# Performance work log

Hardware: AMD Instinct MI355X
Metric: run time of the kernel (lower is better)

## Reference

```python
import jax, jax.numpy as jnp
import numpy as np
from jax import lax

B = 64          # batch
L = 8192        # seq_len
NB = 20         # n_pha_bands + n_amp_bands
K = 769         # padded FIR kernel length (odd), ~cycle*fs/low_hz for lowest band


def setup_inputs() -> dict:
    key = jax.random.key(0)
    kx, kk = jax.random.split(key)
    x = jax.random.normal(kx, (B, 1, L), dtype=jnp.float32)
    # stand-in for the designed+padded tensorpac FIR bank (registered buffer)
    kernels = jax.random.normal(kk, (NB, K), dtype=jnp.float32) * (1.0 / K)
    return {"x": x, "kernels": kernels}


def reference(x, kernels):
    # filtfilt_mode=True, edge_mode=None branch of BandPassFilter.forward
    nb, k = kernels.shape
    seq_len = x.shape[-1]
    padlen = min(3 * k, seq_len - 1)  # same for all bands: kernels share padded length
    xs = x[:, 0, :]  # [B, L]
    # scipy-style odd extension, vectorized over batch (replaces per-sample loop)
    left = -jnp.flip(xs[:, 1:padlen + 1], axis=-1)
    right = -jnp.flip(xs[:, -padlen - 1:-1], axis=-1)
    xp = jnp.concatenate([left, xs, right], axis=-1)[:, None, :]  # [B,1,Lp]
    same = [(k // 2, k // 2)]  # 'same' padding for odd k
    w = kernels[:, None, :]    # [NB,1,K] (OIH)
    dn = ("NCH", "OIH", "NCH")
    # forward pass: all bands at once (replaces per-band loop)
    y = lax.conv_general_dilated(xp, w, (1,), same, dimension_numbers=dn)  # [B,NB,Lp]
    # backward pass of filtfilt: flip, depthwise conv per band, flip back
    y2 = lax.conv_general_dilated(jnp.flip(y, -1), w, (1,), same,
                                  dimension_numbers=dn, feature_group_count=nb)
    y2 = jnp.flip(y2, -1)[:, :, padlen:-padlen]  # crop odd extension -> [B,NB,L]
    return y2[:, None, :, :]  # [B,1,NB,L]
```

## Files before the change

kernel.cpp:

```cpp
#include <hip/hip_runtime.h>

#define B_      64
#define L_      8192
#define NB_     20
#define K_      769
#define GLEN    1537
#define GSM     1552
#define NST3    25
#define NSTP3   28
#define TB      256
#define CPF     1176
#define NWF     1120
#define NWB     1128
#define XB      (8 * CPF)
#define LDS_H   (16 * CPF)
#define CREF    1856
#define PADLEN  2307
#define OFFSET  1539
#define PBUF    (NB_ * GSM)

typedef _Float16 half8  __attribute__((ext_vector_type(8)));
typedef float    f32x4  __attribute__((ext_vector_type(4)));

#define MFMA16(a, b, c) __builtin_amdgcn_mfma_f32_16x16x32_f16((a), (b), (c), 0, 0, 0)

__global__ __launch_bounds__(256) void bp_combine(
    const float* __restrict__ kern, float* __restrict__ gpart)
{
    __shared__ __align__(16) float ks[K_];
    const int o   = blockIdx.x;
    const int jc  = blockIdx.z;
    const int tid = threadIdx.x;
    for (int i = tid; i < K_; i += 256) ks[i] = kern[o * K_ + i];
    __syncthreads();

    const int m = blockIdx.y * 97 + (tid >> 1);
    if (tid < 194 && m < GSM) {
        int jlo = (m > K_ - 1) ? (m - (K_ - 1)) : 0;
        int jhi = (m < K_ - 1) ? m : (K_ - 1);
        if (jlo < jc * 193) jlo = jc * 193;
        if (jhi > jc * 193 + 192) jhi = jc * 193 + 192;
        const int jmid = (jlo + jhi + 1) >> 1;
        const int ja = (tid & 1) ? jmid : jlo;
        const int jb = (tid & 1) ? jhi  : jmid - 1;
        float acc = 0.f;
        for (int j = ja; j <= jb; ++j)
            acc = fmaf(ks[K_ - 1 - j], ks[m - j], acc);
        acc += __shfl_xor(acc, 1);
        if (!(tid & 1)) gpart[jc * PBUF + o * GSM + m] = acc;
    }
}

__global__ __launch_bounds__(256) void bp_pack(
    const float* __restrict__ gpart, _Float16* __restrict__ gbuf)
{
    const int t = blockIdx.x * 256 + threadIdx.x;
    if (t >= NSTP3 * 2 * 64) return;
    const int l    = t & 63;
    const int tau  = (t >> 6) & 1;
    const int step = t >> 7;
    const int g4   = l >> 4;
    const int o    = 16 * tau + (l & 15);
    half8 f;
    #pragma unroll
    for (int e = 0; e < 8; ++e) {
        const int tap = 32 * step + 8 * g4 + e;
        float v = 0.f;
        if (o < NB_ && tap <= 768) {
            const int idx = o * GSM + tap;
            const float gg = gpart[idx] + gpart[PBUF + idx] +
                             gpart[2 * PBUF + idx] + gpart[3 * PBUF + idx];
            v = gg * (tap == 768 ? 512.0f : 1024.0f);
        }
        f[e] = (_Float16)v;
    }
    *((half8*)gbuf + t) = f;
}

__global__ __launch_bounds__(256, 4) void bp_mfma(
    const float* __restrict__ x, const _Float16* __restrict__ gbuf,
    float* __restrict__ out)
{
    __shared__ __align__(16) _Float16 lds[LDS_H];

    const int blk  = blockIdx.x;
    const int tile = blk & 31;
    const int b    = blk >> 5;
    const int tid  = threadIdx.x;
    const int l    = tid & 63;
    const int w    = tid >> 6;

    const int T0 = tile * TB;
    const int P0 = T0 + OFFSET;
    const float* __restrict__ xrow = x + b * L_;

    float fv[5], bv[5];
    #pragma unroll
    for (int r = 0; r < 5; ++r) {
        const int i = tid + 256 * r;
        if (i < NWF) {
            const int p = P0 + i;
            fv[r] = (p < PADLEN) ? -xrow[PADLEN - p]
                  : (p < PADLEN + L_) ? xrow[p - PADLEN]
                  : -xrow[(L_ - 2) + (PADLEN + L_) - p];
        }
        if (i < NWB) {
            const int p2 = P0 + CREF - i;
            bv[r] = (p2 < PADLEN) ? -xrow[PADLEN - p2]
                  : (p2 < PADLEN + L_) ? xrow[p2 - PADLEN]
                  : -xrow[(L_ - 2) + (PADLEN + L_) - p2];
        }
    }
    #pragma unroll
    for (int r = 0; r < 5; ++r) {
        const int i = tid + 256 * r;
        if (i < NWF) {
            const _Float16 h = (_Float16)fv[r];
            #pragma unroll
            for (int cc = 0; cc < 8; ++cc)
                if (i - cc >= 0) lds[cc * CPF + (i - cc)] = h;
        }
        if (i < NWB) {
            const _Float16 h = (_Float16)bv[r];
            #pragma unroll
            for (int cc = 0; cc < 8; ++cc)
                if (i - cc >= 0) lds[XB + cc * CPF + (i - cc)] = h;
        }
    }
    __syncthreads();

    const int g4 = l >> 4;
    const int t4 = l & 15;
    const int cf = l & 7;
    const int cb = (16 - t4) & 7;

    f32x4 acc0[4], acc1[4];
    #pragma unroll
    for (int q = 0; q < 4; ++q) {
        acc0[q] = (f32x4){0.f, 0.f, 0.f, 0.f};
        acc1[q] = (f32x4){0.f, 0.f, 0.f, 0.f};
    }

    const int base_f = 64 * w + t4 + 8 * g4;
    const int base_b = 320 - 64 * w - t4 + 8 * g4;
    const char* lbf0 = (const char*)lds + 2 * (cf * CPF + (base_f - cf));
    const char* lbb0 = (const char*)lds + 2 * (XB + cb * CPF + (base_b - cb));

    half8 R[8], Rb[8];
    #pragma unroll
    for (int a = 0; a < 8; ++a)
        R[a] = *(const half8*)(lbf0 + 32 * a);
    Rb[0] = *(const half8*)(lbb0);
    #pragma unroll
    for (int j = 1; j < 8; ++j)
        Rb[j] = *(const half8*)(lbb0 - 32 * (8 - j));

    const half8* __restrict__ gp = (const half8*)gbuf + l;
    half8 ga[2][2];
    ga[0][0] = gp[0];   ga[0][1] = gp[64];
    ga[1][0] = gp[128]; ga[1][1] = gp[192];

    for (int n = 0; n < 6; ++n) {
        const char* lbf = lbf0 + 256 * n;
        const char* lbb = lbb0 + 256 * n;
        const half8* gpn = gp + 128 * 4 * n;
        #pragma unroll
        for (int k4 = 0; k4 < 4; ++k4) {
            const int p = 2 * k4;
            const int sel = k4 & 1;
            __builtin_amdgcn_s_setprio(1);
            #pragma unroll
            for (int q = 0; q < 4; ++q) {
                const half8 Bq = R[(p + q) & 7] + Rb[(p + 8 - q) & 7];
                acc0[q] = MFMA16(ga[sel][0], Bq, acc0[q]);
                acc1[q] = MFMA16(ga[sel][1], Bq, acc1[q]);
            }
            __builtin_amdgcn_s_setprio(0);
            R[p & 7]        = *(const half8*)(lbf + 64 * k4 + 256);
            R[(p + 1) & 7]  = *(const half8*)(lbf + 64 * k4 + 288);
            Rb[(p + 1) & 7] = *(const half8*)(lbb + 64 * k4 + 32);
            Rb[(p + 2) & 7] = *(const half8*)(lbb + 64 * k4 + 64);
            ga[sel][0] = gpn[(k4 + 2) * 128];
            ga[sel][1] = gpn[(k4 + 2) * 128 + 64];
        }
    }

    __builtin_amdgcn_s_setprio(1);
    #pragma unroll
    for (int q = 0; q < 4; ++q) {
        const half8 Bq = R[q & 7] + Rb[(8 - q) & 7];
        acc0[q] = MFMA16(ga[0][0], Bq, acc0[q]);
        acc1[q] = MFMA16(ga[0][1], Bq, acc1[q]);
    }
    __builtin_amdgcn_s_setprio(0);

    const float sc = 1.0f / 1024.0f;
    #pragma unroll
    for (int q = 0; q < 4; ++q) {
        const int tb = T0 + 64 * w + 16 * q + t4;
        #pragma unroll
        for (int r = 0; r < 4; ++r) {
            const int o0 = 4 * g4 + r;
            __builtin_nontemporal_store(acc0[q][r] * sc,
                                        &out[((b * NB_ + o0) << 13) + tb]);
        }
        if (g4 == 0) {
            #pragma unroll
            for (int r = 0; r < 4; ++r) {
                const int o1 = 16 + r;
                __builtin_nontemporal_store(acc1[q][r] * sc,
                                            &out[((b * NB_ + o1) << 13) + tb]);
            }
        }
    }
}

extern "C" void kernel_launch(void* const* d_in, const int* in_sizes, int n_in,
                              void* d_out, int out_size, void* d_ws, size_t ws_size,
                              hipStream_t stream)
{
    const float* x    = (const float*)d_in[0];
    const float* kern = (const float*)d_in[1];
    float*       out  = (float*)d_out;

    float*    gpart = (float*)d_ws;
    _Float16* gbuf  = (_Float16*)((char*)d_ws + 496640);

    bp_combine<<<dim3(NB_, 16, 4), 256, 0, stream>>>(kern, gpart);
    bp_pack<<<14, 256, 0, stream>>>(gpart, gbuf);
    bp_mfma<<<B_ * (L_ / TB), 256, 0, stream>>>(x, gbuf, out);
}
```

Measured before the change: 42.69 us.

## Precompute reversed fp16 signal in global memory, halve LDS staging for backward taps

```diff
diff --git a/kernel.cpp b/kernel.cpp
--- a/kernel.cpp
+++ b/kernel.cpp
@@ -11,18 +11,22 @@
 #define TB      256
 #define CPF     1176
 #define NWF     1120
-#define NWB     1128
-#define XB      (8 * CPF)
-#define LDS_H   (16 * CPF)
-#define CREF    1856
+#define LDS_H   (8 * CPF)
+#define XRD     4560
+#define XREF    11331
 #define PADLEN  2307
 #define OFFSET  1539
 #define PBUF    (NB_ * GSM)
 
 typedef _Float16 half8  __attribute__((ext_vector_type(8)));
+typedef _Float16 half8u __attribute__((ext_vector_type(8), aligned(4)));
 typedef float    f32x4  __attribute__((ext_vector_type(4)));
 
 #define MFMA16(a, b, c) __builtin_amdgcn_mfma_f32_16x16x32_f16((a), (b), (c), 0, 0, 0)
+
+__device__ __forceinline__ half8 ldg_h8(const char* p) {
+    return (half8)(*(const half8u*)p);
+}
 
 __global__ __launch_bounds__(256) void bp_combine(
     const float* __restrict__ kern, float* __restrict__ gpart)
@@ -77,9 +81,33 @@
     *((half8*)gbuf + t) = f;
 }
 
+__global__ __launch_bounds__(256) void bp_xprep(
+    const float* __restrict__ x, unsigned int* __restrict__ xr)
+{
+    const int b  = blockIdx.x;
+    const int i2 = blockIdx.y * 256 + threadIdx.x;
+    if (i2 >= XRD) return;
+    const float* __restrict__ xrow = x + b * L_;
+    unsigned short h[3];
+    #pragma unroll
+    for (int e = 0; e < 3; ++e) {
+        const int m = 2 * i2 + e;
+        const int p = XREF - m;
+        const float v = (p < PADLEN) ? -xrow[PADLEN - p]
+                      : (p < PADLEN + L_) ? xrow[p - PADLEN]
+                      : -xrow[(L_ - 2) + (PADLEN + L_) - p];
+        union { _Float16 f; unsigned short s; } u;
+        u.f = (_Float16)v;
+        h[e] = u.s;
+    }
+    unsigned int* xrb = xr + (size_t)b * (2 * XRD);
+    xrb[i2]       = ((unsigned int)h[1] << 16) | h[0];
+    xrb[XRD + i2] = ((unsigned int)h[2] << 16) | h[1];
+}
+
 __global__ __launch_bounds__(256, 4) void bp_mfma(
     const float* __restrict__ x, const _Float16* __restrict__ gbuf,
-    float* __restrict__ out)
+    const unsigned int* __restrict__ xr, float* __restrict__ out)
 {
     __shared__ __align__(16) _Float16 lds[LDS_H];
 
@@ -94,7 +122,7 @@
     const int P0 = T0 + OFFSET;
     const float* __restrict__ xrow = x + b * L_;
 
-    float fv[5], bv[5];
+    float fv[5];
     #pragma unroll
     for (int r = 0; r < 5; ++r) {
         const int i = tid + 256 * r;
@@ -104,12 +132,6 @@
                   : (p < PADLEN + L_) ? xrow[p - PADLEN]
                   : -xrow[(L_ - 2) + (PADLEN + L_) - p];
         }
-        if (i < NWB) {
-            const int p2 = P0 + CREF - i;
-            bv[r] = (p2 < PADLEN) ? -xrow[PADLEN - p2]
-                  : (p2 < PADLEN + L_) ? xrow[p2 - PADLEN]
-                  : -xrow[(L_ - 2) + (PADLEN + L_) - p2];
-        }
     }
     #pragma unroll
     for (int r = 0; r < 5; ++r) {
@@ -120,19 +142,12 @@
             for (int cc = 0; cc < 8; ++cc)
                 if (i - cc >= 0) lds[cc * CPF + (i - cc)] = h;
         }
-        if (i < NWB) {
-            const _Float16 h = (_Float16)bv[r];
-            #pragma unroll
-            for (int cc = 0; cc < 8; ++cc)
-                if (i - cc >= 0) lds[XB + cc * CPF + (i - cc)] = h;
-        }
     }
     __syncthreads();
 
     const int g4 = l >> 4;
     const int t4 = l & 15;
     const int cf = l & 7;
-    const int cb = (16 - t4) & 7;
 
     f32x4 acc0[4], acc1[4];
     #pragma unroll
@@ -142,18 +157,23 @@
     }
 
     const int base_f = 64 * w + t4 + 8 * g4;
+    const char* lbf0 = (const char*)lds + 2 * (cf * CPF + (base_f - cf));
+
     const int base_b = 320 - 64 * w - t4 + 8 * g4;
-    const char* lbf0 = (const char*)lds + 2 * (cf * CPF + (base_f - cf));
-    const char* lbb0 = (const char*)lds + 2 * (XB + cb * CPF + (base_b - cb));
+    const int mb0 = (7936 - T0) + base_b;
+    const unsigned int* xrb = xr + (size_t)b * (2 * XRD);
+    const char* gbb0 = (t4 & 1)
+        ? (const char*)(xrb + XRD) + 2 * (mb0 - 1)
+        : (const char*)xrb + 2 * mb0;
 
     half8 R[8], Rb[8];
     #pragma unroll
     for (int a = 0; a < 8; ++a)
         R[a] = *(const half8*)(lbf0 + 32 * a);
-    Rb[0] = *(const half8*)(lbb0);
+    Rb[0] = ldg_h8(gbb0);
     #pragma unroll
     for (int j = 1; j < 8; ++j)
-        Rb[j] = *(const half8*)(lbb0 - 32 * (8 - j));
+        Rb[j] = ldg_h8(gbb0 - 32 * (8 - j));
 
     const half8* __restrict__ gp = (const half8*)gbuf + l;
     half8 ga[2][2];
@@ -162,7 +182,7 @@
 
     for (int n = 0; n < 6; ++n) {
         const char* lbf = lbf0 + 256 * n;
-        const char* lbb = lbb0 + 256 * n;
+        const char* gbb = gbb0 + 256 * n;
         const half8* gpn = gp + 128 * 4 * n;
         #pragma unroll
         for (int k4 = 0; k4 < 4; ++k4) {
@@ -178,8 +198,8 @@
             __builtin_amdgcn_s_setprio(0);
             R[p & 7]        = *(const half8*)(lbf + 64 * k4 + 256);
             R[(p + 1) & 7]  = *(const half8*)(lbf + 64 * k4 + 288);
-            Rb[(p + 1) & 7] = *(const half8*)(lbb + 64 * k4 + 32);
-            Rb[(p + 2) & 7] = *(const half8*)(lbb + 64 * k4 + 64);
+            Rb[(p + 1) & 7] = ldg_h8(gbb + 64 * k4 + 32);
+            Rb[(p + 2) & 7] = ldg_h8(gbb + 64 * k4 + 64);
             ga[sel][0] = gpn[(k4 + 2) * 128];
             ga[sel][1] = gpn[(k4 + 2) * 128 + 64];
         }
@@ -223,10 +243,12 @@
     const float* kern = (const float*)d_in[1];
     float*       out  = (float*)d_out;
 
-    float*    gpart = (float*)d_ws;
-    _Float16* gbuf  = (_Float16*)((char*)d_ws + 496640);
+    float*        gpart = (float*)d_ws;
+    _Float16*     gbuf  = (_Float16*)((char*)d_ws + 496640);
+    unsigned int* xrbuf = (unsigned int*)((char*)d_ws + 557056);
 
     bp_combine<<<dim3(NB_, 16, 4), 256, 0, stream>>>(kern, gpart);
     bp_pack<<<14, 256, 0, stream>>>(gpart, gbuf);
-    bp_mfma<<<B_ * (L_ / TB), 256, 0, stream>>>(x, gbuf, out);
-}
+    bp_xprep<<<dim3(B_, (XRD + 255) / 256), 256, 0, stream>>>(x, xrbuf);
+    bp_mfma<<<B_ * (L_ / TB), 256, 0, stream>>>(x, gbuf, xrbuf, out);
+}
```

Measured after the change: 57.65 us. 35.0% more time.

## Halve shifted LDS copies to 4 using 8-byte split loads, trim combine grid

Applied to the files above, without the earlier changes.

```diff
diff --git a/kernel.cpp b/kernel.cpp
--- a/kernel.cpp
+++ b/kernel.cpp
@@ -12,17 +12,24 @@
 #define CPF     1176
 #define NWF     1120
 #define NWB     1128
-#define XB      (8 * CPF)
-#define LDS_H   (16 * CPF)
+#define XB      (4 * CPF)
+#define LDS_H   (8 * CPF)
 #define CREF    1856
 #define PADLEN  2307
 #define OFFSET  1539
 #define PBUF    (NB_ * GSM)
 
+typedef _Float16 half4  __attribute__((ext_vector_type(4)));
 typedef _Float16 half8  __attribute__((ext_vector_type(8)));
 typedef float    f32x4  __attribute__((ext_vector_type(4)));
 
 #define MFMA16(a, b, c) __builtin_amdgcn_mfma_f32_16x16x32_f16((a), (b), (c), 0, 0, 0)
+
+__device__ __forceinline__ half8 ld_h8(const char* p) {
+    const half4 lo = *(const half4*)p;
+    const half4 hi = *(const half4*)(p + 8);
+    return __builtin_shufflevector(lo, hi, 0, 1, 2, 3, 4, 5, 6, 7);
+}
 
 __global__ __launch_bounds__(256) void bp_combine(
     const float* __restrict__ kern, float* __restrict__ gpart)
@@ -35,9 +42,9 @@
     __syncthreads();
 
     const int m = blockIdx.y * 97 + (tid >> 1);
-    if (tid < 194 && m < GSM) {
-        int jlo = (m > K_ - 1) ? (m - (K_ - 1)) : 0;
-        int jhi = (m < K_ - 1) ? m : (K_ - 1);
+    if (tid < 194 && m <= 768) {
+        int jlo = 0;
+        int jhi = m;
         if (jlo < jc * 193) jlo = jc * 193;
         if (jhi > jc * 193 + 192) jhi = jc * 193 + 192;
         const int jmid = (jlo + jhi + 1) >> 1;
@@ -117,13 +124,13 @@
         if (i < NWF) {
             const _Float16 h = (_Float16)fv[r];
             #pragma unroll
-            for (int cc = 0; cc < 8; ++cc)
+            for (int cc = 0; cc < 4; ++cc)
                 if (i - cc >= 0) lds[cc * CPF + (i - cc)] = h;
         }
         if (i < NWB) {
             const _Float16 h = (_Float16)bv[r];
             #pragma unroll
-            for (int cc = 0; cc < 8; ++cc)
+            for (int cc = 0; cc < 4; ++cc)
                 if (i - cc >= 0) lds[XB + cc * CPF + (i - cc)] = h;
         }
     }
@@ -131,8 +138,8 @@
 
     const int g4 = l >> 4;
     const int t4 = l & 15;
-    const int cf = l & 7;
-    const int cb = (16 - t4) & 7;
+    const int cf = t4 & 3;
+    const int cb = (4 - cf) & 3;
 
     f32x4 acc0[4], acc1[4];
     #pragma unroll
@@ -149,11 +156,11 @@
     half8 R[8], Rb[8];
     #pragma unroll
     for (int a = 0; a < 8; ++a)
-        R[a] = *(const half8*)(lbf0 + 32 * a);
-    Rb[0] = *(const half8*)(lbb0);
+        R[a] = ld_h8(lbf0 + 32 * a);
+    Rb[0] = ld_h8(lbb0);
     #pragma unroll
     for (int j = 1; j < 8; ++j)
-        Rb[j] = *(const half8*)(lbb0 - 32 * (8 - j));
+        Rb[j] = ld_h8(lbb0 - 32 * (8 - j));
 
     const half8* __restrict__ gp = (const half8*)gbuf + l;
     half8 ga[2][2];
@@ -176,10 +183,10 @@
                 acc1[q] = MFMA16(ga[sel][1], Bq, acc1[q]);
             }
             __builtin_amdgcn_s_setprio(0);
-            R[p & 7]        = *(const half8*)(lbf + 64 * k4 + 256);
-            R[(p + 1) & 7]  = *(const half8*)(lbf + 64 * k4 + 288);
-            Rb[(p + 1) & 7] = *(const half8*)(lbb + 64 * k4 + 32);
-            Rb[(p + 2) & 7] = *(const half8*)(lbb + 64 * k4 + 64);
+            R[p & 7]        = ld_h8(lbf + 64 * k4 + 256);
+            R[(p + 1) & 7]  = ld_h8(lbf + 64 * k4 + 288);
+            Rb[(p + 1) & 7] = ld_h8(lbb + 64 * k4 + 32);
+            Rb[(p + 2) & 7] = ld_h8(lbb + 64 * k4 + 64);
             ga[sel][0] = gpn[(k4 + 2) * 128];
             ga[sel][1] = gpn[(k4 + 2) * 128 + 64];
         }
@@ -226,7 +233,7 @@
     float*    gpart = (float*)d_ws;
     _Float16* gbuf  = (_Float16*)((char*)d_ws + 496640);
 
-    bp_combine<<<dim3(NB_, 16, 4), 256, 0, stream>>>(kern, gpart);
+    bp_combine<<<dim3(NB_, 8, 4), 256, 0, stream>>>(kern, gpart);
     bp_pack<<<14, 256, 0, stream>>>(gpart, gbuf);
     bp_mfma<<<B_ * (L_ / TB), 256, 0, stream>>>(x, gbuf, out);
 }
```

Result: slower. 44.89 us (+5.2%).

## Merge filter precompute into one kernel and double MFMA tile to 512 samples

Applied to the files above, without the earlier changes.

```diff
diff --git a/kernel.cpp b/kernel.cpp
--- a/kernel.cpp
+++ b/kernel.cpp
@@ -4,88 +4,69 @@
 #define L_      8192
 #define NB_     20
 #define K_      769
-#define GLEN    1537
-#define GSM     1552
 #define NST3    25
 #define NSTP3   28
-#define TB      256
-#define CPF     1176
-#define NWF     1120
-#define NWB     1128
+#define TB      512
+#define CPF     1432
+#define NWF     1392
 #define XB      (8 * CPF)
 #define LDS_H   (16 * CPF)
-#define CREF    1856
+#define CREF    2112
 #define PADLEN  2307
 #define OFFSET  1539
-#define PBUF    (NB_ * GSM)
 
 typedef _Float16 half8  __attribute__((ext_vector_type(8)));
 typedef float    f32x4  __attribute__((ext_vector_type(4)));
 
 #define MFMA16(a, b, c) __builtin_amdgcn_mfma_f32_16x16x32_f16((a), (b), (c), 0, 0, 0)
 
-__global__ __launch_bounds__(256) void bp_combine(
-    const float* __restrict__ kern, float* __restrict__ gpart)
+__global__ __launch_bounds__(256) void bp_filter(
+    const float* __restrict__ kern, _Float16* __restrict__ gbuf)
 {
     __shared__ __align__(16) float ks[K_];
+    __shared__ __align__(16) float gm[772];
     const int o   = blockIdx.x;
-    const int jc  = blockIdx.z;
     const int tid = threadIdx.x;
-    for (int i = tid; i < K_; i += 256) ks[i] = kern[o * K_ + i];
+
+    if (o < NB_)
+        for (int i = tid; i < K_; i += 256) ks[i] = kern[o * K_ + i];
     __syncthreads();
 
-    const int m = blockIdx.y * 97 + (tid >> 1);
-    if (tid < 194 && m < GSM) {
-        int jlo = (m > K_ - 1) ? (m - (K_ - 1)) : 0;
-        int jhi = (m < K_ - 1) ? m : (K_ - 1);
-        if (jlo < jc * 193) jlo = jc * 193;
-        if (jhi > jc * 193 + 192) jhi = jc * 193 + 192;
-        const int jmid = (jlo + jhi + 1) >> 1;
-        const int ja = (tid & 1) ? jmid : jlo;
-        const int jb = (tid & 1) ? jhi  : jmid - 1;
+    for (int m = tid; m <= 768; m += 256) {
         float acc = 0.f;
-        for (int j = ja; j <= jb; ++j)
-            acc = fmaf(ks[K_ - 1 - j], ks[m - j], acc);
-        acc += __shfl_xor(acc, 1);
-        if (!(tid & 1)) gpart[jc * PBUF + o * GSM + m] = acc;
+        if (o < NB_) {
+            for (int j = 0; j <= m; ++j)
+                acc = fmaf(ks[K_ - 1 - j], ks[m - j], acc);
+            acc *= (m == 768 ? 512.0f : 1024.0f);
+        }
+        gm[m] = acc;
+    }
+    __syncthreads();
+
+    const int tau = o >> 4;
+    const int l15 = o & 15;
+    for (int it = tid; it < NSTP3 * 4; it += 256) {
+        const int S  = it >> 2;
+        const int g4 = it & 3;
+        half8 f;
+        #pragma unroll
+        for (int e = 0; e < 8; ++e) {
+            const int tap = 32 * S + 8 * g4 + e;
+            f[e] = (_Float16)((tap <= 768) ? gm[tap] : 0.f);
+        }
+        *((half8*)gbuf + ((2 * S + tau) * 64 + g4 * 16 + l15)) = f;
     }
 }
 
-__global__ __launch_bounds__(256) void bp_pack(
-    const float* __restrict__ gpart, _Float16* __restrict__ gbuf)
-{
-    const int t = blockIdx.x * 256 + threadIdx.x;
-    if (t >= NSTP3 * 2 * 64) return;
-    const int l    = t & 63;
-    const int tau  = (t >> 6) & 1;
-    const int step = t >> 7;
-    const int g4   = l >> 4;
-    const int o    = 16 * tau + (l & 15);
-    half8 f;
-    #pragma unroll
-    for (int e = 0; e < 8; ++e) {
-        const int tap = 32 * step + 8 * g4 + e;
-        float v = 0.f;
-        if (o < NB_ && tap <= 768) {
-            const int idx = o * GSM + tap;
-            const float gg = gpart[idx] + gpart[PBUF + idx] +
-                             gpart[2 * PBUF + idx] + gpart[3 * PBUF + idx];
-            v = gg * (tap == 768 ? 512.0f : 1024.0f);
-        }
-        f[e] = (_Float16)v;
-    }
-    *((half8*)gbuf + t) = f;
-}
-
-__global__ __launch_bounds__(256, 4) void bp_mfma(
+__global__ __launch_bounds__(512, 4) void bp_mfma(
     const float* __restrict__ x, const _Float16* __restrict__ gbuf,
     float* __restrict__ out)
 {
     __shared__ __align__(16) _Float16 lds[LDS_H];
 
     const int blk  = blockIdx.x;
-    const int tile = blk & 31;
-    const int b    = blk >> 5;
+    const int tile = blk & 15;
+    const int b    = blk >> 4;
     const int tid  = threadIdx.x;
     const int l    = tid & 63;
     const int w    = tid >> 6;
@@ -94,17 +75,15 @@
     const int P0 = T0 + OFFSET;
     const float* __restrict__ xrow = x + b * L_;
 
-    float fv[5], bv[5];
-    #pragma unroll
-    for (int r = 0; r < 5; ++r) {
-        const int i = tid + 256 * r;
+    float fv[3], bv[3];
+    #pragma unroll
+    for (int r = 0; r < 3; ++r) {
+        const int i = tid + 512 * r;
         if (i < NWF) {
             const int p = P0 + i;
             fv[r] = (p < PADLEN) ? -xrow[PADLEN - p]
                   : (p < PADLEN + L_) ? xrow[p - PADLEN]
                   : -xrow[(L_ - 2) + (PADLEN + L_) - p];
-        }
-        if (i < NWB) {
             const int p2 = P0 + CREF - i;
             bv[r] = (p2 < PADLEN) ? -xrow[PADLEN - p2]
                   : (p2 < PADLEN + L_) ? xrow[p2 - PADLEN]
@@ -112,27 +91,26 @@
         }
     }
     #pragma unroll
-    for (int r = 0; r < 5; ++r) {
-        const int i = tid + 256 * r;
+    for (int r = 0; r < 3; ++r) {
+        const int i = tid + 512 * r;
         if (i < NWF) {
-            const _Float16 h = (_Float16)fv[r];
+            const _Float16 hf = (_Float16)fv[r];
+            const _Float16 hb = (_Float16)bv[r];
             #pragma unroll
-            for (int cc = 0; cc < 8; ++cc)
-                if (i - cc >= 0) lds[cc * CPF + (i - cc)] = h;
-        }
-        if (i < NWB) {
-            const _Float16 h = (_Float16)bv[r];
-            #pragma unroll
-            for (int cc = 0; cc < 8; ++cc)
-                if (i - cc >= 0) lds[XB + cc * CPF + (i - cc)] = h;
+            for (int cc = 0; cc < 8; ++cc) {
+                if (i - cc >= 0) {
+                    lds[cc * CPF + (i - cc)] = hf;
+                    lds[XB + cc * CPF + (i - cc)] = hb;
+                }
+            }
         }
     }
     __syncthreads();
 
     const int g4 = l >> 4;
     const int t4 = l & 15;
-    const int cf = l & 7;
-    const int cb = (16 - t4) & 7;
+    const int cf = t4 & 7;
+    const int cb = (-t4) & 7;
 
     f32x4 acc0[4], acc1[4];
     #pragma unroll
@@ -142,7 +120,7 @@
     }
 
     const int base_f = 64 * w + t4 + 8 * g4;
-    const int base_b = 320 - 64 * w - t4 + 8 * g4;
+    const int base_b = 576 - 64 * w - t4 + 8 * g4;
     const char* lbf0 = (const char*)lds + 2 * (cf * CPF + (base_f - cf));
     const char* lbb0 = (const char*)lds + 2 * (XB + cb * CPF + (base_b - cb));
 
@@ -223,10 +201,8 @@
     const float* kern = (const float*)d_in[1];
     float*       out  = (float*)d_out;
 
-    float*    gpart = (float*)d_ws;
-    _Float16* gbuf  = (_Float16*)((char*)d_ws + 496640);
-
-    bp_combine<<<dim3(NB_, 16, 4), 256, 0, stream>>>(kern, gpart);
-    bp_pack<<<14, 256, 0, stream>>>(gpart, gbuf);
-    bp_mfma<<<B_ * (L_ / TB), 256, 0, stream>>>(x, gbuf, out);
+    _Float16* gbuf = (_Float16*)d_ws;
+
+    bp_filter<<<32, 256, 0, stream>>>(kern, gbuf);
+    bp_mfma<<<B_ * (L_ / TB), 512, 0, stream>>>(x, gbuf, out);
 }
```

After: 56.72 us. +32.9%, slower.
